# Performance work log

Measured on AMD Instinct MI355X. Metric: run time of the kernel, lower is better.

Reference implementation:

```python
import jax, jax.numpy as jnp
import numpy as np

N = 50000      # nodes
E = 600000     # edges
D_IN = 5
D_H = 128
EPS = 1e-5     # BatchNorm1d default eps


def batch_norm(x, gamma, beta):
    # training-mode BN over the node dimension (biased variance)
    m = jnp.mean(x, axis=0)
    v = jnp.var(x, axis=0)
    return (x - m) * jax.lax.rsqrt(v + EPS) * gamma + beta


def gcn_conv(x, W, b, src, dst, w):
    # PyG GCNConv: linear transform, add self-loops (weight 1),
    # symmetric normalization D^-1/2 A D^-1/2, scatter-add to dst, + bias.
    x = x @ W                                   # [N, out]
    n = x.shape[0]
    loop = jnp.arange(n)
    src = jnp.concatenate([src, loop])
    dst = jnp.concatenate([dst, loop])
    w = jnp.concatenate([w, jnp.ones((n,), w.dtype)])
    deg = jax.ops.segment_sum(w, dst, num_segments=n)
    dis = jnp.where(deg > 0, jax.lax.rsqrt(jnp.maximum(deg, 1e-12)), 0.0)
    norm = dis[src] * w * dis[dst]              # [E+N]
    msgs = norm[:, None] * x[src]               # gather + scale
    return jax.ops.segment_sum(msgs, dst, num_segments=n) + b


def setup_inputs() -> dict:
    key = jax.random.key(0)
    ks = jax.random.split(key, 20)
    s_in = 1.0 / np.sqrt(D_IN)
    s_h = 1.0 / np.sqrt(D_H)
    return {
        "h": jax.random.normal(ks[0], (N, D_IN), jnp.float32),
        "edge_index": jax.random.randint(ks[1], (2, E), 0, N),
        "edge_weight": jax.random.uniform(ks[2], (E,), jnp.float32),
        "g0": 1.0 + 0.1 * jax.random.normal(ks[3], (D_IN,), jnp.float32),
        "be0": 0.1 * jax.random.normal(ks[4], (D_IN,), jnp.float32),
        "W1": jax.random.normal(ks[5], (D_IN, D_H), jnp.float32) * s_in,
        "b1": jax.random.normal(ks[6], (D_H,), jnp.float32) * s_in,
        "g1": 1.0 + 0.1 * jax.random.normal(ks[7], (D_H,), jnp.float32),
        "be1": 0.1 * jax.random.normal(ks[8], (D_H,), jnp.float32),
        "W2": jax.random.normal(ks[9], (D_H, D_H), jnp.float32) * s_h,
        "b2": jax.random.normal(ks[10], (D_H,), jnp.float32) * s_h,
        "g2": 1.0 + 0.1 * jax.random.normal(ks[11], (D_H,), jnp.float32),
        "be2": 0.1 * jax.random.normal(ks[12], (D_H,), jnp.float32),
        "Wmu": jax.random.normal(ks[13], (D_H, D_H), jnp.float32) * s_h,
        "bmu": jax.random.normal(ks[14], (D_H,), jnp.float32) * s_h,
        "Wls": jax.random.normal(ks[15], (D_H, D_H), jnp.float32) * s_h,
        "bls": jax.random.normal(ks[16], (D_H,), jnp.float32) * s_h,
    }


def reference(h, edge_index, edge_weight, g0, be0, W1, b1, g1, be1,
              W2, b2, g2, be2, Wmu, bmu, Wls, bls):
    src, dst = edge_index[0], edge_index[1]
    h = batch_norm(h, g0, be0)
    h = jax.nn.relu(batch_norm(gcn_conv(h, W1, b1, src, dst, edge_weight), g1, be1))
    # dropout p=0.1 treated as eval-mode (identity)
    h = jax.nn.relu(batch_norm(gcn_conv(h, W2, b2, src, dst, edge_weight), g2, be2))
    mu = h @ Wmu + bmu
    log_std = h @ Wls + bls
    return (mu, log_std)
```

## Files before the change

### kernel.cpp

```cpp
#include <hip/hip_runtime.h>

#define N_NODES 50000
#define N_EDGES 600000
#define D_IN 5
#define D_H 128
#define BN_EPS 1e-5f
#define SCAN_BLOCKS ((N_NODES + 255) / 256)
#define DEG_BLOCKS ((N_EDGES + 255) / 256)
#define FIX_SCALE 16777216.0f
#define FIX_INV   (1.0f / 16777216.0f)

typedef __bf16 bf16x8 __attribute__((ext_vector_type(8)));
typedef float  f32x4  __attribute__((ext_vector_type(4)));

__device__ inline unsigned short f2bfb(float f) {
    unsigned u = __builtin_bit_cast(unsigned, f);
    unsigned r = u + 0x7fffu + ((u >> 16) & 1u);
    return (unsigned short)(r >> 16);
}
__device__ inline float bflo(unsigned u) { return __builtin_bit_cast(float, u << 16); }
__device__ inline float bfhi(unsigned u) { return __builtin_bit_cast(float, u & 0xffff0000u); }

__global__ __launch_bounds__(256) void k_prep(const float* __restrict__ W2,
                                              const float* __restrict__ Wmu,
                                              const float* __restrict__ Wls,
                                              unsigned short* __restrict__ T2,
                                              unsigned short* __restrict__ Tmu,
                                              unsigned short* __restrict__ Tls,
                                              const float* __restrict__ h,
                                              float* __restrict__ stats0,
                                              const int* __restrict__ dst,
                                              const float* __restrict__ w,
                                              unsigned long long* __restrict__ degcnt,
                                              int* __restrict__ rank)
{
    __shared__ float ss[D_IN], sq[D_IN];
    int b = blockIdx.x;
    int t = threadIdx.x;
    if (b < 192) {
        int mat = b >> 6;
        int idx = (b & 63) * 256 + t;
        const float* W = (mat == 0) ? W2 : (mat == 1) ? Wmu : Wls;
        unsigned short* T = (mat == 0) ? T2 : (mat == 1) ? Tmu : Tls;
        int k = idx >> 7, n = idx & 127;
        int fid = (n >> 4) * 4 + (k >> 5);
        int l   = ((k >> 3) & 3) * 16 + (n & 15);
        int j   = k & 7;
        T[fid * 512 + l * 8 + j] = f2bfb(W[idx]);
    } else if (b < 192 + SCAN_BLOCKS) {
        if (t < D_IN) { ss[t] = 0.f; sq[t] = 0.f; }
        __syncthreads();
        int node = (b - 192) * 256 + t;
        float v[D_IN];
#pragma unroll
        for (int f = 0; f < D_IN; ++f)
            v[f] = (node < N_NODES) ? h[node * D_IN + f] : 0.f;
        int lane = t & 63;
#pragma unroll
        for (int f = 0; f < D_IN; ++f) {
            float s = v[f], q = v[f] * v[f];
            for (int off = 32; off > 0; off >>= 1) {
                s += __shfl_down(s, off);
                q += __shfl_down(q, off);
            }
            if (lane == 0) { atomicAdd(&ss[f], s); atomicAdd(&sq[f], q); }
        }
        __syncthreads();
        if (t < D_IN) {
            atomicAdd(&stats0[t], ss[t]);
            atomicAdd(&stats0[D_IN + t], sq[t]);
        }
    } else {
        int e = (b - 192 - SCAN_BLOCKS) * 256 + t;
        if (e < N_EDGES) {
            int d = dst[e];
            unsigned long long fx = (unsigned long long)(w[e] * FIX_SCALE + 0.5f);
            unsigned long long old = atomicAdd(degcnt + d, (1ull << 40) | fx);
            rank[e] = (int)(old >> 40);
        }
    }
}

__global__ __launch_bounds__(256) void k_scan1(const unsigned long long* __restrict__ degcnt,
                                               float* __restrict__ dis,
                                               int* __restrict__ blocksums)
{
    __shared__ int sm[256];
    int t = threadIdx.x;
    int i = blockIdx.x * 256 + t;
    int c = 0;
    if (i < N_NODES) {
        unsigned long long v = degcnt[i];
        c = (int)(v >> 40);
        float deg = (float)(v & ((1ull << 40) - 1)) * FIX_INV;
        dis[i] = rsqrtf(deg + 1.0f);
    }
    sm[t] = c;
    __syncthreads();
    for (int off = 128; off > 0; off >>= 1) {
        if (t < off) sm[t] += sm[t + off];
        __syncthreads();
    }
    if (t == 0) blocksums[blockIdx.x] = sm[0];
}

__global__ __launch_bounds__(256) void k_scan3(const unsigned long long* __restrict__ degcnt,
                                               int* __restrict__ rowptr,
                                               const int* __restrict__ blocksums)
{
    __shared__ int sm[256];
    __shared__ int soff;
    int t = threadIdx.x;
    int bid = blockIdx.x;
    int pre = (t < bid) ? blocksums[t] : 0;
    sm[t] = pre;
    __syncthreads();
    for (int off = 128; off > 0; off >>= 1) {
        if (t < off) sm[t] += sm[t + off];
        __syncthreads();
    }
    if (t == 0) soff = sm[0];
    __syncthreads();
    int i = bid * 256 + t;
    int c = (i < N_NODES) ? (int)(degcnt[i] >> 40) : 0;
    sm[t] = c;
    __syncthreads();
    for (int off = 1; off < 256; off <<= 1) {
        int v = (t >= off) ? sm[t - off] : 0;
        __syncthreads();
        sm[t] += v;
        __syncthreads();
    }
    if (i < N_NODES)
        rowptr[i] = soff + sm[t] - c;
    if (bid == 0 && t == 0)
        rowptr[N_NODES] = N_EDGES;
}

__global__ __launch_bounds__(256) void k_fill(const int* __restrict__ src,
                                              const int* __restrict__ dst,
                                              const float* __restrict__ w,
                                              const float* __restrict__ dis,
                                              const int* __restrict__ rowptr,
                                              const int* __restrict__ rank,
                                              int2* __restrict__ csr)
{
    int e = blockIdx.x * blockDim.x + threadIdx.x;
    if (e < N_EDGES) {
        int s = src[e], d = dst[e];
        float pn = dis[s] * w[e];
        int pos = rowptr[d] + rank[e];
        int2 pk;
        pk.x = s;
        pk.y = __builtin_bit_cast(int, pn);
        csr[pos] = pk;
    }
}

__global__ __launch_bounds__(256) void k_agg0(const float* __restrict__ h,
                                              const float* __restrict__ stats,
                                              const float* __restrict__ g0,
                                              const float* __restrict__ be0,
                                              const int* __restrict__ rowptr,
                                              const int2* __restrict__ csr,
                                              const float* __restrict__ dis,
                                              float* __restrict__ agg,
                                              float* __restrict__ statsA)
{
    __shared__ float sA[20];
    int t = threadIdx.x;
    if (t < 20) sA[t] = 0.f;
    __syncthreads();
    int n = blockIdx.x * 256 + t;
    float av[D_IN] = {0.f, 0.f, 0.f, 0.f, 0.f};
    if (n < N_NODES) {
        float sc[D_IN], sh[D_IN];
#pragma unroll
        for (int f = 0; f < D_IN; ++f) {
            float m = stats[f] * (1.0f / N_NODES);
            float var = stats[D_IN + f] * (1.0f / N_NODES) - m * m;
            sc[f] = rsqrtf(var + BN_EPS) * g0[f];
            sh[f] = be0[f] - m * sc[f];
        }
        float dn = dis[n];
        float acc[D_IN];
#pragma unroll
        for (int f = 0; f < D_IN; ++f)
            acc[f] = dn * (h[n * D_IN + f] * sc[f] + sh[f]);
        int e0 = rowptr[n], e1 = rowptr[n + 1];
        for (int e = e0; e < e1; ++e) {
            int2 pk = csr[e];
            int s = pk.x;
            float pn = __builtin_bit_cast(float, pk.y);
#pragma unroll
            for (int f = 0; f < D_IN; ++f)
                acc[f] += pn * (h[s * D_IN + f] * sc[f] + sh[f]);
        }
#pragma unroll
        for (int f = 0; f < D_IN; ++f) {
            float o = dn * acc[f];
            agg[n * D_IN + f] = o;
            av[f] = o;
        }
    }
    float red[20];
#pragma unroll
    for (int f = 0; f < D_IN; ++f) red[f] = av[f];
    {
        int idx = D_IN;
#pragma unroll
        for (int k = 0; k < D_IN; ++k)
#pragma unroll
            for (int l = k; l < D_IN; ++l)
                red[idx++] = av[k] * av[l];
    }
#pragma unroll
    for (int off = 32; off > 0; off >>= 1) {
#pragma unroll
        for (int i = 0; i < 20; ++i)
            red[i] += __shfl_down(red[i], off);
    }
    if ((t & 63) == 0) {
#pragma unroll
        for (int i = 0; i < 20; ++i)
            atomicAdd(&sA[i], red[i]);
    }
    __syncthreads();
    if (t < 20) atomicAdd(statsA + t, sA[t]);
}

__global__ __launch_bounds__(256) void k_l1(const float* __restrict__ agg,
                                            const float* __restrict__ W1,
                                            const float* __restrict__ b1,
                                            const float* __restrict__ g1,
                                            const float* __restrict__ be1,
                                            const float* __restrict__ statsA,
                                            unsigned short* __restrict__ x)
{
    int t = threadIdx.x;
    int idx0 = blockIdx.x * 256 + t;
    int f0 = (idx0 & 63) * 2;
    float wa[D_IN], wb[D_IN];
#pragma unroll
    for (int k = 0; k < D_IN; ++k) {
        wa[k] = W1[k * D_H + f0];
        wb[k] = W1[k * D_H + f0 + 1];
    }
    float ba = b1[f0], bb = b1[f0 + 1];

    const float inv = 1.0f / N_NODES;
    float S1[D_IN];
#pragma unroll
    for (int k = 0; k < D_IN; ++k) S1[k] = statsA[k];
    float M[D_IN][D_IN];
    {
        int idx = D_IN;
#pragma unroll
        for (int k = 0; k < D_IN; ++k)
#pragma unroll
            for (int l = k; l < D_IN; ++l) {
                float v = statsA[idx++];
                M[k][l] = v;
                M[l][k] = v;
            }
    }
    float t1a = 0.f, t1b = 0.f, qa = 0.f, qb = 0.f;
#pragma unroll
    for (int k = 0; k < D_IN; ++k) { t1a += wa[k] * S1[k]; t1b += wb[k] * S1[k]; }
#pragma unroll
    for (int k = 0; k < D_IN; ++k) {
        float ra = 0.f, rb = 0.f;
#pragma unroll
        for (int l = 0; l < D_IN; ++l) { ra += M[k][l] * wa[l]; rb += M[k][l] * wb[l]; }
        qa += wa[k] * ra;
        qb += wb[k] * rb;
    }
    float ma = t1a * inv, mb = t1b * inv;
    float mua = ma + ba, mub = mb + bb;
    float vara = fmaxf(qa * inv - ma * ma, 0.f);
    float varb = fmaxf(qb * inv - mb * mb, 0.f);
    float sca = rsqrtf(vara + BN_EPS) * g1[f0];
    float scb = rsqrtf(varb + BN_EPS) * g1[f0 + 1];
    float sha = be1[f0] - mua * sca;
    float shb = be1[f0 + 1] - mub * scb;

    const int stride = 512 * 256;
    for (int idx = idx0; idx < N_NODES * 64; idx += stride) {
        int n = idx >> 6;
        const float* a = agg + n * D_IN;
        float v0 = ba, v1 = bb;
#pragma unroll
        for (int k = 0; k < D_IN; ++k) { v0 += wa[k] * a[k]; v1 += wb[k] * a[k]; }
        v0 = fmaxf(v0 * sca + sha, 0.f);
        v1 = fmaxf(v1 * scb + shb, 0.f);
        ((unsigned*)x)[idx] = (unsigned)f2bfb(v0) | ((unsigned)f2bfb(v1) << 16);
    }
}

__global__ __launch_bounds__(256) void k_fused2(const unsigned short* __restrict__ x,
                                                const int* __restrict__ rowptr,
                                                const int2* __restrict__ csr,
                                                const float* __restrict__ dis,
                                                const unsigned short* __restrict__ Bf,
                                                const float* __restrict__ bias,
                                                unsigned short* __restrict__ C,
                                                float* __restrict__ stats)
{
    __shared__ uint4 ldsA[1024];
    __shared__ float sm_s[D_H], sm_q[D_H];
    int t = threadIdx.x;
    if (t < D_H) { sm_s[t] = 0.f; sm_q[t] = 0.f; }
    int m_ = t >> 4;
    int fc = t & 15;
    int f0 = fc * 8;
    int ksw = fc >> 2, quadw = fc & 3;
    int sbase = ksw * 64 + quadw * 16 + m_;
    int gsw = ksw * 2 + (quadw & 1);

    for (int p = 0; p < 4; ++p) {
        int n = blockIdx.x * 64 + p * 16 + m_;
        uint4 o = {0u, 0u, 0u, 0u};
        if (n < N_NODES) {
            float dn = dis[n];
            uint4 hv = *(const uint4*)(x + (size_t)n * D_H + f0);
            float a0 = dn * bflo(hv.x), a1 = dn * bfhi(hv.x);
            float a2 = dn * bflo(hv.y), a3 = dn * bfhi(hv.y);
            float a4 = dn * bflo(hv.z), a5 = dn * bfhi(hv.z);
            float a6 = dn * bflo(hv.w), a7 = dn * bfhi(hv.w);
            int e = rowptr[n], e1 = rowptr[n + 1];
            for (; e + 4 <= e1; e += 4) {
                int2 p0 = csr[e + 0], p1 = csr[e + 1], p2 = csr[e + 2], p3 = csr[e + 3];
                float w0 = __builtin_bit_cast(float, p0.y);
                float w1 = __builtin_bit_cast(float, p1.y);
                float w2 = __builtin_bit_cast(float, p2.y);
                float w3 = __builtin_bit_cast(float, p3.y);
                uint4 v0 = *(const uint4*)(x + (size_t)p0.x * D_H + f0);
                uint4 v1 = *(const uint4*)(x + (size_t)p1.x * D_H + f0);
                uint4 v2 = *(const uint4*)(x + (size_t)p2.x * D_H + f0);
                uint4 v3 = *(const uint4*)(x + (size_t)p3.x * D_H + f0);
                a0 += w0 * bflo(v0.x) + w1 * bflo(v1.x) + w2 * bflo(v2.x) + w3 * bflo(v3.x);
                a1 += w0 * bfhi(v0.x) + w1 * bfhi(v1.x) + w2 * bfhi(v2.x) + w3 * bfhi(v3.x);
                a2 += w0 * bflo(v0.y) + w1 * bflo(v1.y) + w2 * bflo(v2.y) + w3 * bflo(v3.y);
                a3 += w0 * bfhi(v0.y) + w1 * bfhi(v1.y) + w2 * bfhi(v2.y) + w3 * bfhi(v3.y);
                a4 += w0 * bflo(v0.z) + w1 * bflo(v1.z) + w2 * bflo(v2.z) + w3 * bflo(v3.z);
                a5 += w0 * bfhi(v0.z) + w1 * bfhi(v1.z) + w2 * bfhi(v2.z) + w3 * bfhi(v3.z);
                a6 += w0 * bflo(v0.w) + w1 * bflo(v1.w) + w2 * bflo(v2.w) + w3 * bflo(v3.w);
                a7 += w0 * bfhi(v0.w) + w1 * bfhi(v1.w) + w2 * bfhi(v2.w) + w3 * bfhi(v3.w);
            }
            for (; e < e1; ++e) {
                int2 pk = csr[e];
                float pn = __builtin_bit_cast(float, pk.y);
                uint4 v = *(const uint4*)(x + (size_t)pk.x * D_H + f0);
                a0 += pn * bflo(v.x); a1 += pn * bfhi(v.x);
                a2 += pn * bflo(v.y); a3 += pn * bfhi(v.y);
                a4 += pn * bflo(v.z); a5 += pn * bfhi(v.z);
                a6 += pn * bflo(v.w); a7 += pn * bfhi(v.w);
            }
            o.x = (unsigned)f2bfb(dn * a0) | ((unsigned)f2bfb(dn * a1) << 16);
            o.y = (unsigned)f2bfb(dn * a2) | ((unsigned)f2bfb(dn * a3) << 16);
            o.z = (unsigned)f2bfb(dn * a4) | ((unsigned)f2bfb(dn * a5) << 16);
            o.w = (unsigned)f2bfb(dn * a6) | ((unsigned)f2bfb(dn * a7) << 16);
        }
        ldsA[(p * 256 + sbase) ^ gsw] = o;
    }
    __syncthreads();

    int wave = t >> 6, lane = t & 63;
    int m = lane & 15, quad = lane >> 4;
    int r0 = blockIdx.x * 64 + wave * 16;
    bf16x8 af[4];
#pragma unroll
    for (int ks = 0; ks < 4; ++ks) {
        int s = (wave * 4 + ks) * 64 + lane;
        int g = ks * 2 + (quad & 1);
        af[ks] = ((const bf16x8*)ldsA)[s ^ g];
    }
    const bf16x8* bp = (const bf16x8*)Bf;
    f32x4 acc[8];
#pragma unroll
    for (int ct = 0; ct < 8; ++ct) acc[ct] = (f32x4)(0.f);
#pragma unroll
    for (int ks = 0; ks < 4; ++ks) {
#pragma unroll
        for (int ct = 0; ct < 8; ++ct) {
            acc[ct] = __builtin_amdgcn_mfma_f32_16x16x32_bf16(
                af[ks], bp[(ct * 4 + ks) * 64 + lane], acc[ct], 0, 0, 0);
        }
    }
#pragma unroll
    for (int ct = 0; ct < 8; ++ct) {
        int col = ct * 16 + m;
        float bv = bias[col];
        float s = 0.f, q = 0.f;
#pragma unroll
        for (int r = 0; r < 4; ++r) {
            int rr = r0 + quad * 4 + r;
            if (rr < N_NODES) {
                float v = acc[ct][r] + bv;
                C[(size_t)rr * D_H + col] = f2bfb(v);
                s += v; q += v * v;
            }
        }
        atomicAdd(&sm_s[col], s);
        atomicAdd(&sm_q[col], q);
    }
    __syncthreads();
    if (t < D_H) {
        atomicAdd(stats + t, sm_s[t]);
        atomicAdd(stats + D_H + t, sm_q[t]);
    }
}

__global__ __launch_bounds__(256) void k_gemm_out_mf(const unsigned short* __restrict__ A,
                                                     const float* __restrict__ stats,
                                                     const float* __restrict__ g,
                                                     const float* __restrict__ be,
                                                     const unsigned short* __restrict__ Bfmu,
                                                     const float* __restrict__ bmu,
                                                     const unsigned short* __restrict__ Bfls,
                                                     const float* __restrict__ bls,
                                                     float* __restrict__ out)
{
    int t = threadIdx.x;
    int wave = t >> 6, lane = t & 63;
    int m = lane & 15, quad = lane >> 4;
    int r0 = blockIdx.x * 64 + wave * 16;
    int arow = r0 + m < N_NODES ? r0 + m : N_NODES - 1;
    const unsigned short* arowp = A + (size_t)arow * D_H + quad * 8;
    const float inv = 1.0f / N_NODES;
    bf16x8 af[4];
#pragma unroll
    for (int ks = 0; ks < 4; ++ks) {
        uint4 av = *(const uint4*)(arowp + ks * 32);
        float vals[8] = { bflo(av.x), bfhi(av.x), bflo(av.y), bfhi(av.y),
                          bflo(av.z), bfhi(av.z), bflo(av.w), bfhi(av.w) };
        int fb = quad * 8 + ks * 32;
        unsigned short o[8];
#pragma unroll
        for (int j = 0; j < 8; ++j) {
            int f = fb + j;
            float mm = stats[f] * inv;
            float var = stats[D_H + f] * inv - mm * mm;
            float scv = rsqrtf(var + BN_EPS) * g[f];
            float shv = be[f] - mm * scv;
            o[j] = f2bfb(fmaxf(vals[j] * scv + shv, 0.f));
        }
        uint4 pk;
        pk.x = (unsigned)o[0] | ((unsigned)o[1] << 16);
        pk.y = (unsigned)o[2] | ((unsigned)o[3] << 16);
        pk.z = (unsigned)o[4] | ((unsigned)o[5] << 16);
        pk.w = (unsigned)o[6] | ((unsigned)o[7] << 16);
        af[ks] = __builtin_bit_cast(bf16x8, pk);
    }
#pragma unroll
    for (int half = 0; half < 2; ++half) {
        const bf16x8* bp = (const bf16x8*)(half ? Bfls : Bfmu);
        const float* bias = half ? bls : bmu;
        float* C = out + (half ? (size_t)N_NODES * D_H : 0);
        f32x4 acc[8];
#pragma unroll
        for (int ct = 0; ct < 8; ++ct) acc[ct] = (f32x4)(0.f);
#pragma unroll
        for (int ks = 0; ks < 4; ++ks) {
#pragma unroll
            for (int ct = 0; ct < 8; ++ct) {
                acc[ct] = __builtin_amdgcn_mfma_f32_16x16x32_bf16(
                    af[ks], bp[(ct * 4 + ks) * 64 + lane], acc[ct], 0, 0, 0);
            }
        }
#pragma unroll
        for (int ct = 0; ct < 8; ++ct) {
            int col = ct * 16 + m;
            float bv = bias[col];
#pragma unroll
            for (int r = 0; r < 4; ++r) {
                int rr = r0 + quad * 4 + r;
                if (rr < N_NODES)
                    C[(size_t)rr * D_H + col] = acc[ct][r] + bv;
            }
        }
    }
}

extern "C" void kernel_launch(void* const* d_in, const int* in_sizes, int n_in,
                              void* d_out, int out_size, void* d_ws, size_t ws_size,
                              hipStream_t stream)
{
    const float* h   = (const float*)d_in[0];
    const int*   eidx = (const int*)d_in[1];
    const float* ew  = (const float*)d_in[2];
    const float* g0  = (const float*)d_in[3];
    const float* be0 = (const float*)d_in[4];
    const float* W1  = (const float*)d_in[5];
    const float* b1  = (const float*)d_in[6];
    const float* g1  = (const float*)d_in[7];
    const float* be1 = (const float*)d_in[8];
    const float* W2  = (const float*)d_in[9];
    const float* b2  = (const float*)d_in[10];
    const float* g2  = (const float*)d_in[11];
    const float* be2 = (const float*)d_in[12];
    const float* Wmu = (const float*)d_in[13];
    const float* bmu = (const float*)d_in[14];
    const float* Wls = (const float*)d_in[15];
    const float* bls = (const float*)d_in[16];
    const int* srcv = eidx;
    const int* dstv = eidx + N_EDGES;
    float* out = (float*)d_out;

    char* ws = (char*)d_ws;
    size_t off = 0;
    auto alloc = [&](size_t bytes) -> char* {
        char* p = ws + off;
        off += (bytes + 255) & ~(size_t)255;
        return p;
    };
    float* stats0  = (float*)alloc(16 * 4);
    float* statsA  = (float*)alloc(32 * 4);
    float* stats2  = (float*)alloc(256 * 4);
    unsigned long long* degcnt = (unsigned long long*)alloc(N_NODES * 8);
    size_t zero_bytes = off;
    int*   rowptr  = (int*)  alloc((N_NODES + 1) * 4);
    float* dis     = (float*)alloc(N_NODES * 4);
    int*   rank    = (int*)  alloc((size_t)N_EDGES * 4);
    int*   blocksums = (int*)alloc(256 * 4);
    int2*  csr     = (int2*) alloc((size_t)N_EDGES * 8);
    float* agg0    = (float*)alloc(N_NODES * D_IN * 4);
    unsigned short* x1h  = (unsigned short*)alloc((size_t)N_NODES * D_H * 2);
    unsigned short* c2h  = (unsigned short*)alloc((size_t)N_NODES * D_H * 2);
    unsigned short* Wt2   = (unsigned short*)alloc(D_H * D_H * 2);
    unsigned short* Wtmu  = (unsigned short*)alloc(D_H * D_H * 2);
    unsigned short* Wtls  = (unsigned short*)alloc(D_H * D_H * 2);
    (void)ws_size; (void)in_sizes; (void)n_in; (void)out_size;

    hipMemsetAsync(d_ws, 0, zero_bytes, stream);

    k_prep<<<192 + SCAN_BLOCKS + DEG_BLOCKS, 256, 0, stream>>>(
        W2, Wmu, Wls, Wt2, Wtmu, Wtls, h, stats0, dstv, ew, degcnt, rank);
    k_scan1<<<SCAN_BLOCKS, 256, 0, stream>>>(degcnt, dis, blocksums);
    k_scan3<<<SCAN_BLOCKS, 256, 0, stream>>>(degcnt, rowptr, blocksums);
    k_fill<<<DEG_BLOCKS, 256, 0, stream>>>(srcv, dstv, ew, dis, rowptr, rank, csr);
    k_agg0<<<SCAN_BLOCKS, 256, 0, stream>>>(h, stats0, g0, be0, rowptr, csr, dis,
                                            agg0, statsA);
    k_l1<<<512, 256, 0, stream>>>(agg0, W1, b1, g1, be1, statsA, x1h);
    k_fused2<<<(N_NODES + 63) / 64, 256, 0, stream>>>(x1h, rowptr, csr, dis,
                                                      Wt2, b2, c2h, stats2);
    k_gemm_out_mf<<<(N_NODES + 63) / 64, 256, 0, stream>>>(c2h, stats2, g2, be2,
                                                           Wtmu, bmu, Wtls, bls, out);
}
```

Measured before the change: 269.8 us.

## Split fused layer-2 aggregation+GEMM into separate gather and MFMA GEMM kernels

Replaces the fused kernel that gathered neighbor features into LDS and then ran MFMA with two kernels: a gather kernel using 16 nodes per block, and a GEMM kernel that reads A fragments straight from global memory. The intent is to raise gather parallelism and occupancy, since the fused kernel serialized four gather passes per block and held LDS. In exchange it adds a 12.8 MB bf16 intermediate write and read, plus an extra launch.

```diff
diff --git a/kernel.cpp b/kernel.cpp
--- a/kernel.cpp
+++ b/kernel.cpp
@@ -297,84 +297,76 @@
     }
 }
 
-__global__ __launch_bounds__(256) void k_fused2(const unsigned short* __restrict__ x,
+__global__ __launch_bounds__(256) void k_agg128(const unsigned short* __restrict__ x,
                                                 const int* __restrict__ rowptr,
                                                 const int2* __restrict__ csr,
                                                 const float* __restrict__ dis,
-                                                const unsigned short* __restrict__ Bf,
-                                                const float* __restrict__ bias,
-                                                unsigned short* __restrict__ C,
-                                                float* __restrict__ stats)
-{
-    __shared__ uint4 ldsA[1024];
+                                                unsigned short* __restrict__ outb)
+{
+    int t = threadIdx.x;
+    int n = blockIdx.x * 16 + (t >> 4);
+    int f0 = (t & 15) * 8;
+    if (n >= N_NODES) return;
+    float dn = dis[n];
+    uint4 hv = *(const uint4*)(x + (size_t)n * D_H + f0);
+    float a0 = dn * bflo(hv.x), a1 = dn * bfhi(hv.x);
+    float a2 = dn * bflo(hv.y), a3 = dn * bfhi(hv.y);
+    float a4 = dn * bflo(hv.z), a5 = dn * bfhi(hv.z);
+    float a6 = dn * bflo(hv.w), a7 = dn * bfhi(hv.w);
+    int e = rowptr[n], e1 = rowptr[n + 1];
+    for (; e + 4 <= e1; e += 4) {
+        int2 p0 = csr[e + 0], p1 = csr[e + 1], p2 = csr[e + 2], p3 = csr[e + 3];
+        float w0 = __builtin_bit_cast(float, p0.y);
+        float w1 = __builtin_bit_cast(float, p1.y);
+        float w2 = __builtin_bit_cast(float, p2.y);
+        float w3 = __builtin_bit_cast(float, p3.y);
+        uint4 v0 = *(const uint4*)(x + (size_t)p0.x * D_H + f0);
+        uint4 v1 = *(const uint4*)(x + (size_t)p1.x * D_H + f0);
+        uint4 v2 = *(const uint4*)(x + (size_t)p2.x * D_H + f0);
+        uint4 v3 = *(const uint4*)(x + (size_t)p3.x * D_H + f0);
+        a0 += w0 * bflo(v0.x) + w1 * bflo(v1.x) + w2 * bflo(v2.x) + w3 * bflo(v3.x);
+        a1 += w0 * bfhi(v0.x) + w1 * bfhi(v1.x) + w2 * bfhi(v2.x) + w3 * bfhi(v3.x);
+        a2 += w0 * bflo(v0.y) + w1 * bflo(v1.y) + w2 * bflo(v2.y) + w3 * bflo(v3.y);
+        a3 += w0 * bfhi(v0.y) + w1 * bfhi(v1.y) + w2 * bfhi(v2.y) + w3 * bfhi(v3.y);
+        a4 += w0 * bflo(v0.z) + w1 * bflo(v1.z) + w2 * bflo(v2.z) + w3 * bflo(v3.z);
+        a5 += w0 * bfhi(v0.z) + w1 * bfhi(v1.z) + w2 * bfhi(v2.z) + w3 * bfhi(v3.z);
+        a6 += w0 * bflo(v0.w) + w1 * bflo(v1.w) + w2 * bflo(v2.w) + w3 * bflo(v3.w);
+        a7 += w0 * bfhi(v0.w) + w1 * bfhi(v1.w) + w2 * bfhi(v2.w) + w3 * bfhi(v3.w);
+    }
+    for (; e < e1; ++e) {
+        int2 pk = csr[e];
+        float pn = __builtin_bit_cast(float, pk.y);
+        uint4 v = *(const uint4*)(x + (size_t)pk.x * D_H + f0);
+        a0 += pn * bflo(v.x); a1 += pn * bfhi(v.x);
+        a2 += pn * bflo(v.y); a3 += pn * bfhi(v.y);
+        a4 += pn * bflo(v.z); a5 += pn * bfhi(v.z);
+        a6 += pn * bflo(v.w); a7 += pn * bfhi(v.w);
+    }
+    uint4 o;
+    o.x = (unsigned)f2bfb(dn * a0) | ((unsigned)f2bfb(dn * a1) << 16);
+    o.y = (unsigned)f2bfb(dn * a2) | ((unsigned)f2bfb(dn * a3) << 16);
+    o.z = (unsigned)f2bfb(dn * a4) | ((unsigned)f2bfb(dn * a5) << 16);
+    o.w = (unsigned)f2bfb(dn * a6) | ((unsigned)f2bfb(dn * a7) << 16);
+    *(uint4*)(outb + (size_t)n * D_H + f0) = o;
+}
+
+__global__ __launch_bounds__(256) void k_gemm_mf(const unsigned short* __restrict__ A,
+                                                 const unsigned short* __restrict__ Bf,
+                                                 const float* __restrict__ bias,
+                                                 unsigned short* __restrict__ C,
+                                                 float* __restrict__ stats)
+{
     __shared__ float sm_s[D_H], sm_q[D_H];
     int t = threadIdx.x;
     if (t < D_H) { sm_s[t] = 0.f; sm_q[t] = 0.f; }
-    int m_ = t >> 4;
-    int fc = t & 15;
-    int f0 = fc * 8;
-    int ksw = fc >> 2, quadw = fc & 3;
-    int sbase = ksw * 64 + quadw * 16 + m_;
-    int gsw = ksw * 2 + (quadw & 1);
-
-    for (int p = 0; p < 4; ++p) {
-        int n = blockIdx.x * 64 + p * 16 + m_;
-        uint4 o = {0u, 0u, 0u, 0u};
-        if (n < N_NODES) {
-            float dn = dis[n];
-            uint4 hv = *(const uint4*)(x + (size_t)n * D_H + f0);
-            float a0 = dn * bflo(hv.x), a1 = dn * bfhi(hv.x);
-            float a2 = dn * bflo(hv.y), a3 = dn * bfhi(hv.y);
-            float a4 = dn * bflo(hv.z), a5 = dn * bfhi(hv.z);
-            float a6 = dn * bflo(hv.w), a7 = dn * bfhi(hv.w);
-            int e = rowptr[n], e1 = rowptr[n + 1];
-            for (; e + 4 <= e1; e += 4) {
-                int2 p0 = csr[e + 0], p1 = csr[e + 1], p2 = csr[e + 2], p3 = csr[e + 3];
-                float w0 = __builtin_bit_cast(float, p0.y);
-                float w1 = __builtin_bit_cast(float, p1.y);
-                float w2 = __builtin_bit_cast(float, p2.y);
-                float w3 = __builtin_bit_cast(float, p3.y);
-                uint4 v0 = *(const uint4*)(x + (size_t)p0.x * D_H + f0);
-                uint4 v1 = *(const uint4*)(x + (size_t)p1.x * D_H + f0);
-                uint4 v2 = *(const uint4*)(x + (size_t)p2.x * D_H + f0);
-                uint4 v3 = *(const uint4*)(x + (size_t)p3.x * D_H + f0);
-                a0 += w0 * bflo(v0.x) + w1 * bflo(v1.x) + w2 * bflo(v2.x) + w3 * bflo(v3.x);
-                a1 += w0 * bfhi(v0.x) + w1 * bfhi(v1.x) + w2 * bfhi(v2.x) + w3 * bfhi(v3.x);
-                a2 += w0 * bflo(v0.y) + w1 * bflo(v1.y) + w2 * bflo(v2.y) + w3 * bflo(v3.y);
-                a3 += w0 * bfhi(v0.y) + w1 * bfhi(v1.y) + w2 * bfhi(v2.y) + w3 * bfhi(v3.y);
-                a4 += w0 * bflo(v0.z) + w1 * bflo(v1.z) + w2 * bflo(v2.z) + w3 * bflo(v3.z);
-                a5 += w0 * bfhi(v0.z) + w1 * bfhi(v1.z) + w2 * bfhi(v2.z) + w3 * bfhi(v3.z);
-                a6 += w0 * bflo(v0.w) + w1 * bflo(v1.w) + w2 * bflo(v2.w) + w3 * bflo(v3.w);
-                a7 += w0 * bfhi(v0.w) + w1 * bfhi(v1.w) + w2 * bfhi(v2.w) + w3 * bfhi(v3.w);
-            }
-            for (; e < e1; ++e) {
-                int2 pk = csr[e];
-                float pn = __builtin_bit_cast(float, pk.y);
-                uint4 v = *(const uint4*)(x + (size_t)pk.x * D_H + f0);
-                a0 += pn * bflo(v.x); a1 += pn * bfhi(v.x);
-                a2 += pn * bflo(v.y); a3 += pn * bfhi(v.y);
-                a4 += pn * bflo(v.z); a5 += pn * bfhi(v.z);
-                a6 += pn * bflo(v.w); a7 += pn * bfhi(v.w);
-            }
-            o.x = (unsigned)f2bfb(dn * a0) | ((unsigned)f2bfb(dn * a1) << 16);
-            o.y = (unsigned)f2bfb(dn * a2) | ((unsigned)f2bfb(dn * a3) << 16);
-            o.z = (unsigned)f2bfb(dn * a4) | ((unsigned)f2bfb(dn * a5) << 16);
-            o.w = (unsigned)f2bfb(dn * a6) | ((unsigned)f2bfb(dn * a7) << 16);
-        }
-        ldsA[(p * 256 + sbase) ^ gsw] = o;
-    }
-    __syncthreads();
-
     int wave = t >> 6, lane = t & 63;
     int m = lane & 15, quad = lane >> 4;
     int r0 = blockIdx.x * 64 + wave * 16;
+    int arow = r0 + m < N_NODES ? r0 + m : N_NODES - 1;
+    const bf16x8* ap = (const bf16x8*)(A + (size_t)arow * D_H + quad * 8);
     bf16x8 af[4];
 #pragma unroll
-    for (int ks = 0; ks < 4; ++ks) {
-        int s = (wave * 4 + ks) * 64 + lane;
-        int g = ks * 2 + (quad & 1);
-        af[ks] = ((const bf16x8*)ldsA)[s ^ g];
-    }
+    for (int ks = 0; ks < 4; ++ks) af[ks] = ap[ks * 4];
     const bf16x8* bp = (const bf16x8*)Bf;
     f32x4 acc[8];
 #pragma unroll
@@ -387,6 +379,7 @@
                 af[ks], bp[(ct * 4 + ks) * 64 + lane], acc[ct], 0, 0, 0);
         }
     }
+    __syncthreads();
 #pragma unroll
     for (int ct = 0; ct < 8; ++ct) {
         int col = ct * 16 + m;
@@ -526,6 +519,7 @@
     int2*  csr     = (int2*) alloc((size_t)N_EDGES * 8);
     float* agg0    = (float*)alloc(N_NODES * D_IN * 4);
     unsigned short* x1h  = (unsigned short*)alloc((size_t)N_NODES * D_H * 2);
+    unsigned short* aggh = (unsigned short*)alloc((size_t)N_NODES * D_H * 2);
     unsigned short* c2h  = (unsigned short*)alloc((size_t)N_NODES * D_H * 2);
     unsigned short* Wt2   = (unsigned short*)alloc(D_H * D_H * 2);
     unsigned short* Wtmu  = (unsigned short*)alloc(D_H * D_H * 2);
@@ -542,8 +536,8 @@
     k_agg0<<<SCAN_BLOCKS, 256, 0, stream>>>(h, stats0, g0, be0, rowptr, csr, dis,
                                             agg0, statsA);
     k_l1<<<512, 256, 0, stream>>>(agg0, W1, b1, g1, be1, statsA, x1h);
-    k_fused2<<<(N_NODES + 63) / 64, 256, 0, stream>>>(x1h, rowptr, csr, dis,
-                                                      Wt2, b2, c2h, stats2);
+    k_agg128<<<(N_NODES + 15) / 16, 256, 0, stream>>>(x1h, rowptr, csr, dis, aggh);
+    k_gemm_mf<<<(N_NODES + 63) / 64, 256, 0, stream>>>(aggh, Wt2, b2, c2h, stats2);
     k_gemm_out_mf<<<(N_NODES + 63) / 64, 256, 0, stream>>>(c2h, stats2, g2, be2,
                                                            Wtmu, bmu, Wtls, bls, out);
 }
```

New measurement: 276.0 us. +2.3%, slower.
